# Optimization experiments

Hardware: AMD Instinct MI355X
Metric: run time of the kernel (lower is better)

## Reference

```python
import jax, jax.numpy as jnp
import numpy as np
import math

N, C_S, C_Z, C_IPA, H, NQ, NV = 768, 384, 128, 16, 12, 4, 8


def setup_inputs() -> dict:
    key = jax.random.key(0)
    ks = jax.random.split(key, 16)
    inp = {
        "s": jax.random.normal(ks[0], (N, C_S), jnp.float32),
        "z": jax.random.normal(ks[1], (N, N, C_Z), jnp.float32),
        "rots": jax.random.normal(ks[2], (N, 3, 3), jnp.float32),
        "trans": jax.random.normal(ks[3], (N, 3), jnp.float32),
        "mask": jnp.ones((N,), jnp.float32),
    }
    sc = 0.02
    inp["Wq"] = jax.random.normal(ks[4], (C_S, H * C_IPA), jnp.float32) * sc
    inp["bq"] = jnp.zeros((H * C_IPA,), jnp.float32)
    inp["Wkv"] = jax.random.normal(ks[5], (C_S, H * 2 * C_IPA), jnp.float32) * sc
    inp["bkv"] = jnp.zeros((H * 2 * C_IPA,), jnp.float32)
    inp["Wq3"] = jax.random.normal(ks[6], (C_S, H * 3 * NQ), jnp.float32) * sc
    inp["bq3"] = jnp.zeros((H * 3 * NQ,), jnp.float32)
    inp["Wkv3"] = jax.random.normal(ks[7], (C_S, H * 3 * (NQ + NV)), jnp.float32) * sc
    inp["bkv3"] = jnp.zeros((H * 3 * (NQ + NV),), jnp.float32)
    inp["Wb"] = jax.random.normal(ks[8], (C_Z, H), jnp.float32) * sc
    inp["bb"] = jnp.zeros((H,), jnp.float32)
    inp["hw"] = jnp.zeros((H,), jnp.float32)
    inp["Wo"] = jax.random.normal(ks[9], (H * (C_Z + C_IPA + NV * 4), C_S), jnp.float32) * sc
    inp["bo"] = jnp.zeros((C_S,), jnp.float32)
    return inp


def reference(s, z, rots, trans, mask, Wq, bq, Wkv, bkv, Wq3, bq3, Wkv3, bkv3, Wb, bb, hw, Wo, bo):
    normsize = math.sqrt(1.0 / (3 * C_IPA))
    normsize_B = math.sqrt(1.0 / 3.0)
    normsize_hw = math.sqrt(1.0 / (3 * NQ * 9.0 / 2))

    # scalar Q/K/V: [N, H, C_IPA]
    Q = (s @ Wq + bq).reshape(N, H, C_IPA)
    KV = (s @ Wkv + bkv).reshape(N, H, 2, C_IPA)
    K, V = KV[..., 0, :], KV[..., 1, :]

    # query points: project, place into global frame via rigid transform
    Q3 = (s @ Wq3 + bq3).reshape(N, 3, NQ * H).swapaxes(-1, -2)        # [N, NQ*H, 3]
    Q3 = jnp.einsum('nij,nkj->nki', rots, Q3) + trans[:, None, :]
    Q3 = Q3.reshape(N, H, NQ, 3)

    KV3 = (s @ Wkv3 + bkv3).reshape(N, 3, H * (NQ + NV)).swapaxes(-1, -2)
    KV3 = jnp.einsum('nij,nkj->nki', rots, KV3) + trans[:, None, :]
    KV3 = KV3.reshape(N, H, NQ + NV, 3)
    K3, V3 = KV3[:, :, :NQ, :], KV3[:, :, NQ:, :]                      # points per head

    # pair bias [N, N, H]
    B = z @ Wb + bb

    # scalar attention logits + pair bias
    AT = jnp.einsum('ihc,jhc->ijh', Q, K) * normsize + B * normsize_B

    # point attention: squared distances [N, N, H, NQ]
    d2 = jnp.sum(jnp.square(Q3[:, None] - K3[None, :]), axis=-1)
    hw_sp = jax.nn.softplus(hw) * normsize_hw                          # [H]
    AT3 = -0.5 * jnp.sum(d2 * hw_sp[None, None, :, None], axis=-1)     # [N, N, H]

    # mask bias: large negative where either residue masked out
    mask2 = mask[:, None] * mask[None, :]
    B3 = (mask2 - 1.0) * 1e9                                           # [N, N]

    AT = jax.nn.softmax(AT + AT3 + B3[..., None], axis=-2)             # softmax over j

    # scalar value aggregation
    O = jnp.einsum('ijh,jhc->ihc', AT, V).reshape(N, -1)

    # point value aggregation, then map back to local frame (inverse transform)
    O3 = jnp.einsum('ijh,jhcd->ihcd', AT, V3).reshape(N, H * NV, 3)
    O3 = jnp.einsum('nji,nkj->nki', rots, O3 - trans[:, None, :])      # rots^T @ (O3 - t)
    O3_norm = jnp.sqrt(jnp.sum(jnp.square(O3), axis=-1) + 1e-20)       # [N, H*NV]

    # pair representation aggregation
    O_pair = jnp.einsum('ijh,ijc->ihc', AT, z).reshape(N, -1)

    O_final = jnp.concatenate((O, O3[..., 0], O3[..., 1], O3[..., 2], O3_norm, O_pair), axis=-1)
    return O_final @ Wo + bo
```

## Files before the change

kernel.cpp:

```cpp
#include <hip/hip_runtime.h>
#include <cstdint>


typedef __attribute__((ext_vector_type(8))) short short8;
typedef __attribute__((ext_vector_type(4))) short short4_t;
typedef __attribute__((ext_vector_type(4))) float f32x4;

__device__ __forceinline__ unsigned short f2bf(float f) {
    unsigned u = __float_as_uint(f);
    u = (u + 0x7FFFu + ((u >> 16) & 1u)) >> 16;
    return (unsigned short)u;
}
__device__ __forceinline__ float bf2f(unsigned short s) {
    return __uint_as_float(((unsigned)s) << 16);
}
__device__ __forceinline__ unsigned pk2(float lo, float hi) {
    return (unsigned)f2bf(lo) | ((unsigned)f2bf(hi) << 16);
}
__device__ __forceinline__ int HOFF(int gg) {
    return gg * 6 + ((gg & 2) << 2);
}

__global__ __launch_bounds__(256) void proj_kernel(
    const float* __restrict__ s,
    const float* __restrict__ Wq,   const float* __restrict__ bq,
    const float* __restrict__ Wkv,  const float* __restrict__ bkv,
    const float* __restrict__ Wq3,  const float* __restrict__ bq3,
    const float* __restrict__ Wkv3, const float* __restrict__ bkv3,
    float* __restrict__ Qw, unsigned short* __restrict__ Kw,
    unsigned short* __restrict__ Vw,
    float* __restrict__ P3q, float* __restrict__ P3kv)
{
    __shared__ __align__(16) float s_lds[32 * 384];
    const int t  = threadIdx.x;
    const int r0 = blockIdx.x * 32;
    const int c0 = blockIdx.y * 128;

    for (int u = t; u < 3072; u += 256) {
        int r = u / 96, c4 = u - r * 96;
        *(float4*)&s_lds[r * 384 + c4 * 4] =
            *(const float4*)&s[(size_t)(r0 + r) * 384 + c4 * 4];
    }
    __syncthreads();

    const int rg = t >> 6;
    const int lc = t & 63;
    const int colA = c0 + lc;
    const int colB = c0 + lc + 64;

    const float *wpA, *wpB; int ldA, ldB; float biasA, biasB;
    {
        int col = colA;
        if (col < 192)      { wpA = Wq   + col;       ldA = 192; biasA = bq[col]; }
        else if (col < 576) { wpA = Wkv  + (col-192); ldA = 384; biasA = bkv[col-192]; }
        else if (col < 720) { wpA = Wq3  + (col-576); ldA = 144; biasA = bq3[col-576]; }
        else                { wpA = Wkv3 + (col-720); ldA = 432; biasA = bkv3[col-720]; }
        col = colB;
        if (col < 192)      { wpB = Wq   + col;       ldB = 192; biasB = bq[col]; }
        else if (col < 576) { wpB = Wkv  + (col-192); ldB = 384; biasB = bkv[col-192]; }
        else if (col < 720) { wpB = Wq3  + (col-576); ldB = 144; biasB = bq3[col-576]; }
        else                { wpB = Wkv3 + (col-720); ldB = 432; biasB = bkv3[col-720]; }
    }

    float acc0[8] = {}, acc1[8] = {};
    for (int k = 0; k < 384; k += 4) {
        float4 sv[8];
        #pragma unroll
        for (int r = 0; r < 8; r++)
            sv[r] = *(const float4*)&s_lds[(rg*8 + r) * 384 + k];
        #pragma unroll
        for (int kk = 0; kk < 4; kk++) {
            float w0 = wpA[(k + kk) * ldA];
            float w1 = wpB[(k + kk) * ldB];
            #pragma unroll
            for (int r = 0; r < 8; r++) {
                float sval = ((const float*)&sv[r])[kk];
                acc0[r] += sval * w0;
                acc1[r] += sval * w1;
            }
        }
    }

    #pragma unroll
    for (int q = 0; q < 2; q++) {
        int col   = q ? colB : colA;
        float bia = q ? biasB : biasA;
        #pragma unroll
        for (int r = 0; r < 8; r++) {
            int row = r0 + rg*8 + r;
            float v = (q ? acc1[r] : acc0[r]) + bia;
            if (col < 192) {
                Qw[(size_t)row*192 + col] = v;
            } else if (col < 576) {
                int c = col - 192, h = c >> 5, sub = c & 31;
                if (sub < 16) Kw[(size_t)row*192 + h*16 + sub]      = f2bf(v);
                else          Vw[(size_t)row*192 + h*16 + (sub-16)] = f2bf(v);
            } else if (col < 720) {
                P3q[(size_t)row*144 + (col-576)] = v;
            } else {
                P3kv[(size_t)row*432 + (col-720)] = v;
            }
        }
    }
}

__global__ __launch_bounds__(192) void rot3_kernel(
    const float* __restrict__ P3q, const float* __restrict__ P3kv,
    const float* __restrict__ rots, const float* __restrict__ trans,
    float* __restrict__ Q3w, unsigned short* __restrict__ K3w,
    unsigned short* __restrict__ V3w)
{
    const int n = blockIdx.x;
    const int t = threadIdx.x;
    float R[9];
    #pragma unroll
    for (int u = 0; u < 9; u++) R[u] = rots[n*9 + u];
    float T0 = trans[n*3+0], T1 = trans[n*3+1], T2 = trans[n*3+2];

    float p0, p1, p2;
    if (t < 48) {
        p0 = P3q[(size_t)n*144 + t];
        p1 = P3q[(size_t)n*144 + 48 + t];
        p2 = P3q[(size_t)n*144 + 96 + t];
    } else {
        int k = t - 48;
        p0 = P3kv[(size_t)n*432 + k];
        p1 = P3kv[(size_t)n*432 + 144 + k];
        p2 = P3kv[(size_t)n*432 + 288 + k];
    }
    float o0 = R[0]*p0 + R[1]*p1 + R[2]*p2 + T0;
    float o1 = R[3]*p0 + R[4]*p1 + R[5]*p2 + T1;
    float o2 = R[6]*p0 + R[7]*p1 + R[8]*p2 + T2;

    if (t < 48) {
        Q3w[(size_t)n*144 + t*3 + 0] = o0;
        Q3w[(size_t)n*144 + t*3 + 1] = o1;
        Q3w[(size_t)n*144 + t*3 + 2] = o2;
    } else {
        int k = t - 48, h = k / 12, m = k % 12;
        if (m < 4) {
            size_t base = (size_t)n*144 + (h*4 + m)*3;
            K3w[base+0] = f2bf(o0); K3w[base+1] = f2bf(o1); K3w[base+2] = f2bf(o2);
        } else {
            size_t base = (size_t)n*384 + (h*8 + (m-4))*4;
            V3w[base+0] = f2bf(o0); V3w[base+1] = f2bf(o1); V3w[base+2] = f2bf(o2);
        }
    }
}

__global__ __launch_bounds__(256, 4) void ipa_main(
    const float* __restrict__ z, const float* __restrict__ mask,
    const float* __restrict__ Wb, const float* __restrict__ bb,
    const float* __restrict__ hw,
    const float* __restrict__ Qw, const unsigned short* __restrict__ Kw,
    const unsigned short* __restrict__ Vw,
    const float* __restrict__ Q3w, const unsigned short* __restrict__ K3w,
    const unsigned short* __restrict__ V3w,
    float* __restrict__ part3)
{
    __shared__ __align__(16) unsigned short z_l[90 * 88];
    __shared__ __align__(16) unsigned short wbT_l[16 * 136];
    __shared__ __align__(16) float          p_l[32 * 17];
    __shared__ __align__(16) unsigned short pT_l[16 * 40];
    __shared__ __align__(16) float          Q_lds[192];
    __shared__ __align__(16) float          Q3_lds[144];
    __shared__ float hw_lds[12], bb_lds[12];

    const int i     = blockIdx.x >> 1;
    const int chunk = blockIdx.x & 1;
    const int t    = threadIdx.x;
    const int lane = t & 63;
    const int wv   = t >> 6;
    const int g    = lane >> 4;
    const int lm   = lane & 15;

    if (t < 192) Q_lds[t]  = Qw[(size_t)i*192 + t];
    if (t < 144) Q3_lds[t] = Q3w[(size_t)i*144 + t];
    if (t < 12) {
        hw_lds[t] = log1pf(__expf(hw[t])) * 0.13608276348795434f;
        bb_lds[t] = bb[t];
    }
    if (t < 160) pT_l[480 + t] = 0;
    for (int u = t; u < 1536; u += 256) {
        int h = u % 12, c = u / 12;
        wbT_l[h*136 + c] = f2bf(Wb[c*12 + h]);
    }
    const float mask_i = mask[i];

    f32x4 opA = {0,0,0,0}, opB = {0,0,0,0};
    float oacc = 0.0f;
    float o3x = 0, o3y = 0, o3z = 0;
    float dena = 0;
    const int oh = t >> 4, oc = t & 15;
    int o3h = -1, o3v = 0, o3j0 = 0, o3j1 = 32, o3slot = 0;
    if (t >= 192)    { o3h = (t - 192) >> 3;      o3v = (t - 192) & 7; }
    else if (t < 32) { o3h = 8 + (t >> 3);        o3v = t & 7;        o3j1 = 16; }
    else if (t < 64) { o3h = 8 + ((t - 32) >> 3); o3v = (t - 32) & 7; o3j0 = 16; o3slot = 1; }
    const int denh = (t >= 64 && t < 76) ? (t - 64) : -1;

    const int jj  = t >> 3, c16 = t & 7;
    const float* zbase = z + ((size_t)i*768 + chunk*384 + jj)*128 + c16*16;
    const int chS  = (jj >> 2)*8 + c16;
    const int chP  = chS + HOFF(chS >> 4);
    const int sidx = chP*88 + (jj & 3)*16;

    __syncthreads();

    for (int tile = 0; tile < 12; tile++) {
        const int j0 = chunk*384 + tile*32;

        {
            const float* zp = zbase + (size_t)tile * 32 * 128;
            float4 f0 = *(const float4*)(zp + 0);
            float4 f1 = *(const float4*)(zp + 4);
            float4 f2 = *(const float4*)(zp + 8);
            float4 f3 = *(const float4*)(zp + 12);
            uint4* dst = (uint4*)&z_l[sidx];
            dst[0] = uint4{pk2(f0.x,f0.y), pk2(f0.z,f0.w), pk2(f1.x,f1.y), pk2(f1.z,f1.w)};
            dst[1] = uint4{pk2(f2.x,f2.y), pk2(f2.z,f2.w), pk2(f3.x,f3.y), pk2(f3.z,f3.w)};
        }
        __syncthreads();

        if (wv < 2) {
            f32x4 ab = {0,0,0,0};
            const int jt = wv;
            #pragma unroll
            for (int ks = 0; ks < 4; ks++) {
                short8 bf = *(const short8*)&wbT_l[lm*136 + ks*32 + g*8];
                int jr = jt*16 + lm;
                int ch = (jr >> 2)*8 + ks*2 + (g >> 1);
                int cp = ch + HOFF(ch >> 4);
                short8 a = *(const short8*)&z_l[cp*88 + (jr & 3)*16 + (g & 1)*8];
                ab = __builtin_amdgcn_mfma_f32_16x16x32_bf16(a, bf, ab, 0, 0, 0);
            }
            if (lm < 12) {
                #pragma unroll
                for (int r = 0; r < 4; r++)
                    p_l[(jt*16 + g*4 + r)*17 + lm] = ab[r];
            }
        }
        __syncthreads();

        #pragma unroll
        for (int rep = 0; rep < 2; rep++) {
            int pr = t + rep*256;
            if (pr < 384) {
                int jjq = pr / 12;
                int h   = pr - jjq*12;
                int j   = j0 + jjq;
                float Bv = p_l[jjq*17 + h];
                const unsigned short* kp = Kw + (size_t)j*192 + h*16;
                short8 kA = *(const short8*)(kp);
                short8 kB = *(const short8*)(kp + 8);
                float qk = 0.0f;
                #pragma unroll
                for (int e = 0; e < 8; e++) qk += Q_lds[h*16 + e]     * bf2f((unsigned short)kA[e]);
                #pragma unroll
                for (int e = 0; e < 8; e++) qk += Q_lds[h*16 + 8 + e] * bf2f((unsigned short)kB[e]);
                const unsigned short* k3p = K3w + (size_t)j*144 + h*12;
                short4_t c0v = *(const short4_t*)(k3p);
                short4_t c1v = *(const short4_t*)(k3p + 4);
                short4_t c2v = *(const short4_t*)(k3p + 8);
                float d2 = 0.0f;
                #pragma unroll
                for (int e = 0; e < 4; e++) { float d = Q3_lds[h*12 + e]     - bf2f((unsigned short)c0v[e]); d2 += d*d; }
                #pragma unroll
                for (int e = 0; e < 4; e++) { float d = Q3_lds[h*12 + 4 + e] - bf2f((unsigned short)c1v[e]); d2 += d*d; }
                #pragma unroll
                for (int e = 0; e < 4; e++) { float d = Q3_lds[h*12 + 8 + e] - bf2f((unsigned short)c2v[e]); d2 += d*d; }
                float mj = mask[j];
                float lg = qk * 0.14433756729740643f
                         + (Bv + bb_lds[h]) * 0.5773502691896258f
                         - 0.5f * hw_lds[h] * d2
                         + (mask_i * mj - 1.0f) * 1e9f;
                float p = __expf(lg);
                p_l[jjq*17 + h]  = p;
                pT_l[h*40 + jjq] = f2bf(p);
            }
        }
        __syncthreads();

        {
            const int nt0 = wv*2;
            short8 ap = *(const short8*)((const char*)pT_l + lm*80 + g*16);
            short8 b0, b1;
            #pragma unroll
            for (int e = 0; e < 8; e++) {
                int jje = g*8 + e;
                int su  = (jje >> 2)*8;
                int ro  = (jje & 3)*16;
                int cp0 = su + nt0 + HOFF(g);
                b0[e] = (short)z_l[cp0*88 + ro + lm];
                b1[e] = (short)z_l[(cp0 + 1)*88 + ro + lm];
            }
            opA = __builtin_amdgcn_mfma_f32_16x16x32_bf16(ap, b0, opA, 0, 0, 0);
            opB = __builtin_amdgcn_mfma_f32_16x16x32_bf16(ap, b1, opB, 0, 0, 0);
        }
        if (t < 192) {
            #pragma unroll 8
            for (int jjq = 0; jjq < 32; jjq++) {
                float p = p_l[jjq*17 + oh];
                oacc += p * bf2f(Vw[(size_t)(j0 + jjq)*192 + oh*16 + oc]);
            }
        }
        if (o3h >= 0) {
            #pragma unroll 8
            for (int jjq = o3j0; jjq < o3j1; jjq++) {
                float p = p_l[jjq*17 + o3h];
                short4_t v4 = *(const short4_t*)(V3w + (size_t)(j0 + jjq)*384 + (o3h*8 + o3v)*4);
                o3x += p * bf2f((unsigned short)v4[0]);
                o3y += p * bf2f((unsigned short)v4[1]);
                o3z += p * bf2f((unsigned short)v4[2]);
            }
        }
        if (denh >= 0) {
            #pragma unroll 8
            for (int jjq = 0; jjq < 32; jjq++) dena += p_l[jjq*17 + denh];
        }
        __syncthreads();
    }

    float* pb = part3 + (size_t)blockIdx.x * 2560;
    if (t < 192) pb[t] = oacc;
    if (o3h >= 0) {
        int base = 192 + o3slot*288 + (o3h*8 + o3v)*3;
        pb[base+0] = o3x; pb[base+1] = o3y; pb[base+2] = o3z;
    }
    if (denh >= 0) pb[2304 + denh] = dena;
    {
        const int nt0 = wv*2;
        #pragma unroll
        for (int r = 0; r < 4; r++) {
            int h = g*4 + r;
            if (h < 12) {
                pb[768 + h*128 + nt0*16 + lm]       = opA[r];
                pb[768 + h*128 + (nt0 + 1)*16 + lm] = opB[r];
            }
        }
    }
}

__global__ __launch_bounds__(256) void combine_kernel(
    const float* __restrict__ part3, const float* __restrict__ rots,
    const float* __restrict__ trans, unsigned short* __restrict__ OF)
{
    const int i = blockIdx.x;
    const int t = threadIdx.x;
    const float* pa = part3 + (size_t)i*2*2560;
    const float* pb = pa + 2560;
    __shared__ float den_s[12];
    if (t < 12) den_s[t] = pa[2304 + t] + pb[2304 + t];
    __syncthreads();

    const size_t ofb = (size_t)i * 2112;
    if (t < 192) OF[ofb + t] = f2bf((pa[t] + pb[t]) / den_s[t >> 4]);
    if (t < 96) {
        int h = t >> 3, v = t & 7;
        float den = den_s[h];
        int base = 192 + t*3;
        float m0 = pa[base+0] + pb[base+0];
        float m1 = pa[base+1] + pb[base+1];
        float m2 = pa[base+2] + pb[base+2];
        if (h >= 8) {
            m0 += pa[base+288+0] + pb[base+288+0];
            m1 += pa[base+288+1] + pb[base+288+1];
            m2 += pa[base+288+2] + pb[base+288+2];
        }
        m0 = m0 / den - trans[i*3+0];
        m1 = m1 / den - trans[i*3+1];
        m2 = m2 / den - trans[i*3+2];
        const float* R = rots + (size_t)i*9;
        float r0v = R[0]*m0 + R[3]*m1 + R[6]*m2;
        float r1v = R[1]*m0 + R[4]*m1 + R[7]*m2;
        float r2v = R[2]*m0 + R[5]*m1 + R[8]*m2;
        float nrm = sqrtf(r0v*r0v + r1v*r1v + r2v*r2v + 1e-20f);
        int hv = h*8 + v;
        OF[ofb + 192 + hv] = f2bf(r0v);
        OF[ofb + 288 + hv] = f2bf(r1v);
        OF[ofb + 384 + hv] = f2bf(r2v);
        OF[ofb + 480 + hv] = f2bf(nrm);
    }
    for (int u = t; u < 1536; u += 256) {
        OF[ofb + 576 + u] = f2bf((pa[768 + u] + pb[768 + u]) / den_s[u >> 7]);
    }
}

__global__ __launch_bounds__(256) void out_gemm(
    const unsigned short* __restrict__ OF, const float* __restrict__ Wo,
    float* __restrict__ part)
{
    __shared__ __align__(16) float aT[32 * 132];
    __shared__ __align__(16) float bt[32 * 68];
    const int t  = threadIdx.x;
    const int i0 = blockIdx.x * 128;
    const int c0 = blockIdx.y * 64;
    const int k0 = blockIdx.z * 352;
    const int r0 = (t & 15) * 8;
    const int c4 = (t >> 4) * 4;

    float acc[8][4] = {};

    for (int kt = 0; kt < 11; kt++) {
        const int kk0 = k0 + kt*32;
        __syncthreads();
        {
            int r = t >> 1, kh = (t & 1) * 16;
            const unsigned short* apg = OF + (size_t)(i0 + r)*2112 + kk0 + kh;
            short8 v0 = *(const short8*)apg;
            short8 v1 = *(const short8*)(apg + 8);
            #pragma unroll
            for (int e = 0; e < 8; e++) aT[(kh + e)*132 + r]     = bf2f((unsigned short)v0[e]);
            #pragma unroll
            for (int e = 0; e < 8; e++) aT[(kh + 8 + e)*132 + r] = bf2f((unsigned short)v1[e]);
        }
        {
            int k = t >> 3, c8 = (t & 7) * 8;
            const float* wpg = Wo + (size_t)(kk0 + k)*384 + c0 + c8;
            *(float4*)&bt[k*68 + c8]     = *(const float4*)wpg;
            *(float4*)&bt[k*68 + c8 + 4] = *(const float4*)(wpg + 4);
        }
        __syncthreads();
        #pragma unroll 4
        for (int kk = 0; kk < 32; kk++) {
            float4 a0 = *(float4*)&aT[kk*132 + r0];
            float4 a1 = *(float4*)&aT[kk*132 + r0 + 4];
            float4 bv = *(float4*)&bt[kk*68 + c4];
            #pragma unroll
            for (int ci = 0; ci < 4; ci++) {
                float b = ((const float*)&bv)[ci];
                acc[0][ci] += ((const float*)&a0)[0] * b;
                acc[1][ci] += ((const float*)&a0)[1] * b;
                acc[2][ci] += ((const float*)&a0)[2] * b;
                acc[3][ci] += ((const float*)&a0)[3] * b;
                acc[4][ci] += ((const float*)&a1)[0] * b;
                acc[5][ci] += ((const float*)&a1)[1] * b;
                acc[6][ci] += ((const float*)&a1)[2] * b;
                acc[7][ci] += ((const float*)&a1)[3] * b;
            }
        }
    }

    float* pbv = part + (size_t)blockIdx.z * 294912;
    #pragma unroll
    for (int ri = 0; ri < 8; ri++) {
        float4 o = {acc[ri][0], acc[ri][1], acc[ri][2], acc[ri][3]};
        *(float4*)&pbv[(size_t)(i0 + r0 + ri)*384 + c0 + c4] = o;
    }
}

__global__ __launch_bounds__(256) void reduce_out(
    const float* __restrict__ part, const float* __restrict__ bo,
    float* __restrict__ out)
{
    int idx = blockIdx.x * 256 + threadIdx.x;
    float v = bo[idx % 384];
    #pragma unroll
    for (int s = 0; s < 6; s++) v += part[(size_t)s * 294912 + idx];
    out[idx] = v;
}

extern "C" void kernel_launch(void* const* d_in, const int* in_sizes, int n_in,
                              void* d_out, int out_size, void* d_ws, size_t ws_size,
                              hipStream_t stream) {
    const float* s     = (const float*)d_in[0];
    const float* z     = (const float*)d_in[1];
    const float* rots  = (const float*)d_in[2];
    const float* trans = (const float*)d_in[3];
    const float* mask  = (const float*)d_in[4];
    const float* Wq    = (const float*)d_in[5];
    const float* bq    = (const float*)d_in[6];
    const float* Wkv   = (const float*)d_in[7];
    const float* bkv   = (const float*)d_in[8];
    const float* Wq3   = (const float*)d_in[9];
    const float* bq3   = (const float*)d_in[10];
    const float* Wkv3  = (const float*)d_in[11];
    const float* bkv3  = (const float*)d_in[12];
    const float* Wb    = (const float*)d_in[13];
    const float* bb    = (const float*)d_in[14];
    const float* hw    = (const float*)d_in[15];
    const float* Wo    = (const float*)d_in[16];
    const float* bo    = (const float*)d_in[17];
    float* out = (float*)d_out;

    char* ws = (char*)d_ws;
    float*          Qw   = (float*)(ws + 0);
    float*          Q3w  = (float*)(ws + 589824);
    unsigned short* Kw   = (unsigned short*)(ws + 1032192);
    unsigned short* Vw   = (unsigned short*)(ws + 1327104);
    unsigned short* K3w  = (unsigned short*)(ws + 1622016);
    unsigned short* V3w  = (unsigned short*)(ws + 1843200);
    float*          P3q  = (float*)(ws + 2433024);
    float*          P3kv = (float*)(ws + 2875392);
    unsigned short* OF   = (unsigned short*)(ws + 4202496);
    float*          part3 = (float*)(ws + 7446528);
    float*          part  = (float*)(ws + 7446528);

    proj_kernel<<<dim3(24, 9), 256, 0, stream>>>(
        s, Wq, bq, Wkv, bkv, Wq3, bq3, Wkv3, bkv3, Qw, Kw, Vw, P3q, P3kv);
    rot3_kernel<<<768, 192, 0, stream>>>(P3q, P3kv, rots, trans, Q3w, K3w, V3w);
    ipa_main<<<1536, 256, 0, stream>>>(
        z, mask, Wb, bb, hw, Qw, Kw, Vw, Q3w, K3w, V3w, part3);
    combine_kernel<<<768, 256, 0, stream>>>(part3, rots, trans, OF);
    out_gemm<<<dim3(6, 6, 6), 256, 0, stream>>>(OF, Wo, part);
    reduce_out<<<1152, 256, 0, stream>>>(part, bo, out);
}
```

Measured before the change: 258.4 us.

## Fold logits into augmented Q/K dot product and pipeline z tiles with V aggregation

Adds an ek_kernel that builds 32-wide augmented query and key rows. Each row packs the scaled scalar q/k, the weighted point coordinates, the squared-norm terms, the bias and the mask terms, so each logit becomes a single dot product instead of separate qk, distance and mask evaluations. V and V3 are stored transposed so each thread reads contiguous j-runs. The main loop prefetches the next z tile into registers and runs the V/V3 aggregation for the previous tile on waves 2-3 while waves 0-1 compute the bias MFMA and the exponentials, using double-buffered probability buffers. The costs are an extra kernel launch, bf16 rounding of the augmented terms, and a mask encoded as a large bf16 constant whose error tolerance depends on S.

After: 473.0 us. 1.83x slower.

```diff
diff --git a/kernel.cpp b/kernel.cpp
--- a/kernel.cpp
+++ b/kernel.cpp
@@ -20,6 +20,10 @@
 __device__ __forceinline__ int HOFF(int gg) {
     return gg * 6 + ((gg & 2) << 2);
 }
+
+#define NS_QK  0.14433756729740643f
+#define NS_B   0.5773502691896258f
+#define NS_HW  0.13608276348795434f
 
 __global__ __launch_bounds__(256) void proj_kernel(
     const float* __restrict__ s,
@@ -28,7 +32,7 @@
     const float* __restrict__ Wq3,  const float* __restrict__ bq3,
     const float* __restrict__ Wkv3, const float* __restrict__ bkv3,
     float* __restrict__ Qw, unsigned short* __restrict__ Kw,
-    unsigned short* __restrict__ Vw,
+    unsigned short* __restrict__ Vt,
     float* __restrict__ P3q, float* __restrict__ P3kv)
 {
     __shared__ __align__(16) float s_lds[32 * 384];
@@ -93,8 +97,8 @@
                 Qw[(size_t)row*192 + col] = v;
             } else if (col < 576) {
                 int c = col - 192, h = c >> 5, sub = c & 31;
-                if (sub < 16) Kw[(size_t)row*192 + h*16 + sub]      = f2bf(v);
-                else          Vw[(size_t)row*192 + h*16 + (sub-16)] = f2bf(v);
+                if (sub < 16) Kw[(size_t)row*192 + h*16 + sub] = f2bf(v);
+                else          Vt[(size_t)(h*16 + (sub-16))*768 + row] = f2bf(v);
             } else if (col < 720) {
                 P3q[(size_t)row*144 + (col-576)] = v;
             } else {
@@ -107,8 +111,8 @@
 __global__ __launch_bounds__(192) void rot3_kernel(
     const float* __restrict__ P3q, const float* __restrict__ P3kv,
     const float* __restrict__ rots, const float* __restrict__ trans,
-    float* __restrict__ Q3w, unsigned short* __restrict__ K3w,
-    unsigned short* __restrict__ V3w)
+    float* __restrict__ Q3w, float* __restrict__ K3w,
+    unsigned short* __restrict__ V3t)
 {
     const int n = blockIdx.x;
     const int t = threadIdx.x;
@@ -140,31 +144,85 @@
         int k = t - 48, h = k / 12, m = k % 12;
         if (m < 4) {
             size_t base = (size_t)n*144 + (h*4 + m)*3;
-            K3w[base+0] = f2bf(o0); K3w[base+1] = f2bf(o1); K3w[base+2] = f2bf(o2);
+            K3w[base+0] = o0; K3w[base+1] = o1; K3w[base+2] = o2;
         } else {
-            size_t base = (size_t)n*384 + (h*8 + (m-4))*4;
-            V3w[base+0] = f2bf(o0); V3w[base+1] = f2bf(o1); V3w[base+2] = f2bf(o2);
-        }
+            int rv = (h*8 + (m-4))*3;
+            V3t[(size_t)(rv+0)*768 + n] = f2bf(o0);
+            V3t[(size_t)(rv+1)*768 + n] = f2bf(o1);
+            V3t[(size_t)(rv+2)*768 + n] = f2bf(o2);
+        }
+    }
+}
+
+__global__ __launch_bounds__(256) void ek_kernel(
+    const float* __restrict__ Qw, const unsigned short* __restrict__ Kw,
+    const float* __restrict__ Q3w, const float* __restrict__ K3w,
+    const float* __restrict__ mask, const float* __restrict__ hw,
+    const float* __restrict__ bb,
+    unsigned short* __restrict__ EQw, unsigned short* __restrict__ EKw)
+{
+    const int idx = blockIdx.x * 4 + (threadIdx.x >> 6);
+    const int h   = threadIdx.x & 63;
+    if (h >= 12) return;
+    const float hws = log1pf(__expf(hw[h])) * NS_HW;
+    const float mi  = mask[idx];
+    const float S   = 31616.0f;
+
+    unsigned short row[32];
+    {
+        const unsigned short* kp = Kw + (size_t)idx*192 + h*16;
+        #pragma unroll
+        for (int c = 0; c < 16; c++) row[c] = kp[c];
+        const float* k3 = K3w + (size_t)idx*144 + h*12;
+        float kn = 0.0f;
+        #pragma unroll
+        for (int e = 0; e < 12; e++) {
+            unsigned short b = f2bf(k3[e]);
+            row[16+e] = b;
+            float f = bf2f(b); kn += f*f;
+        }
+        row[28] = f2bf(bb[h]*NS_B - 0.5f*hws*kn);
+        row[29] = f2bf(1.0f);
+        row[30] = f2bf(mi * S);
+        row[31] = f2bf(-S);
+        unsigned short* o = EKw + ((size_t)idx*12 + h)*32;
+        #pragma unroll
+        for (int c = 0; c < 32; c++) o[c] = row[c];
+    }
+    {
+        const float* qp = Qw + (size_t)idx*192 + h*16;
+        #pragma unroll
+        for (int c = 0; c < 16; c++) row[c] = f2bf(qp[c] * NS_QK);
+        const float* q3 = Q3w + (size_t)idx*144 + h*12;
+        float qn = 0.0f;
+        #pragma unroll
+        for (int e = 0; e < 12; e++) {
+            float f = q3[e];
+            row[16+e] = f2bf(f * hws);
+            qn += f*f;
+        }
+        row[28] = f2bf(1.0f);
+        row[29] = f2bf(-0.5f*hws*qn);
+        row[30] = f2bf(mi * S);
+        row[31] = f2bf(S);
+        unsigned short* o = EQw + ((size_t)idx*12 + h)*32;
+        #pragma unroll
+        for (int c = 0; c < 32; c++) o[c] = row[c];
     }
 }
 
 __global__ __launch_bounds__(256, 4) void ipa_main(
-    const float* __restrict__ z, const float* __restrict__ mask,
-    const float* __restrict__ Wb, const float* __restrict__ bb,
-    const float* __restrict__ hw,
-    const float* __restrict__ Qw, const unsigned short* __restrict__ Kw,
-    const unsigned short* __restrict__ Vw,
-    const float* __restrict__ Q3w, const unsigned short* __restrict__ K3w,
-    const unsigned short* __restrict__ V3w,
+    const float* __restrict__ z,
+    const float* __restrict__ Wb,
+    const unsigned short* __restrict__ EQw, const unsigned short* __restrict__ EKw,
+    const unsigned short* __restrict__ Vt, const unsigned short* __restrict__ V3t,
     float* __restrict__ part3)
 {
     __shared__ __align__(16) unsigned short z_l[90 * 88];
+    __shared__ __align__(16) float          p_l[2][32 * 17];
+    __shared__ __align__(16) unsigned short pT_l[2][16 * 40];
+    __shared__ __align__(16) float          eq_l[12 * 33];
     __shared__ __align__(16) unsigned short wbT_l[16 * 136];
-    __shared__ __align__(16) float          p_l[32 * 17];
-    __shared__ __align__(16) unsigned short pT_l[16 * 40];
-    __shared__ __align__(16) float          Q_lds[192];
-    __shared__ __align__(16) float          Q3_lds[144];
-    __shared__ float hw_lds[12], bb_lds[12];
 
     const int i     = blockIdx.x >> 1;
     const int chunk = blockIdx.x & 1;
@@ -174,29 +232,17 @@
     const int g    = lane >> 4;
     const int lm   = lane & 15;
 
-    if (t < 192) Q_lds[t]  = Qw[(size_t)i*192 + t];
-    if (t < 144) Q3_lds[t] = Q3w[(size_t)i*144 + t];
-    if (t < 12) {
-        hw_lds[t] = log1pf(__expf(hw[t])) * 0.13608276348795434f;
-        bb_lds[t] = bb[t];
-    }
-    if (t < 160) pT_l[480 + t] = 0;
+    for (int u = t; u < 384; u += 256) {
+        int h = u >> 5, c = u & 31;
+        eq_l[h*33 + c] = bf2f(EQw[((size_t)i*12 + h)*32 + c]);
+    }
     for (int u = t; u < 1536; u += 256) {
         int h = u % 12, c = u / 12;
         wbT_l[h*136 + c] = f2bf(Wb[c*12 + h]);
     }
-    const float mask_i = mask[i];
-
-    f32x4 opA = {0,0,0,0}, opB = {0,0,0,0};
-    float oacc = 0.0f;
-    float o3x = 0, o3y = 0, o3z = 0;
-    float dena = 0;
-    const int oh = t >> 4, oc = t & 15;
-    int o3h = -1, o3v = 0, o3j0 = 0, o3j1 = 32, o3slot = 0;
-    if (t >= 192)    { o3h = (t - 192) >> 3;      o3v = (t - 192) & 7; }
-    else if (t < 32) { o3h = 8 + (t >> 3);        o3v = t & 7;        o3j1 = 16; }
-    else if (t < 64) { o3h = 8 + ((t - 32) >> 3); o3v = (t - 32) & 7; o3j0 = 16; o3slot = 1; }
-    const int denh = (t >= 64 && t < 76) ? (t - 64) : -1;
+    for (int u = t; u < 512; u += 256)
+        wbT_l[(12 + (u >> 7))*136 + (u & 127)] = 0;
+    if (t < 160) { pT_l[0][480 + t] = 0; pT_l[1][480 + t] = 0; }
 
     const int jj  = t >> 3, c16 = t & 7;
     const float* zbase = z + ((size_t)i*768 + chunk*384 + jj)*128 + c16*16;
@@ -204,85 +250,137 @@
     const int chP  = chS + HOFF(chS >> 4);
     const int sidx = chP*88 + (jj & 3)*16;
 
+    f32x4 opA = {0,0,0,0}, opB = {0,0,0,0};
+    float oa = 0, ob = 0, oc2 = 0;
+    float o3x = 0, o3y = 0, o3z = 0;
+    float dn = 0;
+    const int w = t - 128;
+
+    {
+        float4 f0 = *(const float4*)(zbase + 0);
+        float4 f1 = *(const float4*)(zbase + 4);
+        float4 f2 = *(const float4*)(zbase + 8);
+        float4 f3 = *(const float4*)(zbase + 12);
+        uint4* dst = (uint4*)&z_l[sidx];
+        dst[0] = uint4{pk2(f0.x,f0.y), pk2(f0.z,f0.w), pk2(f1.x,f1.y), pk2(f1.z,f1.w)};
+        dst[1] = uint4{pk2(f2.x,f2.y), pk2(f2.z,f2.w), pk2(f3.x,f3.y), pk2(f3.z,f3.w)};
+    }
     __syncthreads();
 
+    auto vwork = [&](int tt) {
+        const int j0v = chunk*384 + tt*32;
+        const float* pp = p_l[tt & 1];
+        if (w < 96) {
+            short8 va[4];
+            #pragma unroll
+            for (int q = 0; q < 4; q++)
+                va[q] = *(const short8*)(Vt + (size_t)w*768 + j0v + q*8);
+            short8 v3[3][4];
+            #pragma unroll
+            for (int d = 0; d < 3; d++)
+                #pragma unroll
+                for (int q = 0; q < 4; q++)
+                    v3[d][q] = *(const short8*)(V3t + (size_t)(w*3 + d)*768 + j0v + q*8);
+            const int ohp = w >> 4, o3hp = w >> 3;
+            #pragma unroll
+            for (int j2 = 0; j2 < 32; j2++) {
+                float p1 = pp[j2*17 + ohp];
+                oa += p1 * bf2f((unsigned short)va[j2>>3][j2&7]);
+                float pv = pp[j2*17 + o3hp];
+                o3x += pv * bf2f((unsigned short)v3[0][j2>>3][j2&7]);
+                o3y += pv * bf2f((unsigned short)v3[1][j2>>3][j2&7]);
+                o3z += pv * bf2f((unsigned short)v3[2][j2>>3][j2&7]);
+            }
+        } else {
+            short8 va[4], vb[4], vc[4];
+            #pragma unroll
+            for (int q = 0; q < 4; q++) {
+                va[q] = *(const short8*)(Vt + (size_t)w*768      + j0v + q*8);
+                vb[q] = *(const short8*)(Vt + (size_t)(w+32)*768 + j0v + q*8);
+                vc[q] = *(const short8*)(Vt + (size_t)(w+64)*768 + j0v + q*8);
+            }
+            const int ha = w >> 4, hb = ha + 2, hc = ha + 4;
+            #pragma unroll
+            for (int j2 = 0; j2 < 32; j2++) {
+                oa  += pp[j2*17 + ha] * bf2f((unsigned short)va[j2>>3][j2&7]);
+                ob  += pp[j2*17 + hb] * bf2f((unsigned short)vb[j2>>3][j2&7]);
+                oc2 += pp[j2*17 + hc] * bf2f((unsigned short)vc[j2>>3][j2&7]);
+            }
+        }
+    };
+
     for (int tile = 0; tile < 12; tile++) {
-        const int j0 = chunk*384 + tile*32;
-
-        {
-            const float* zp = zbase + (size_t)tile * 32 * 128;
-            float4 f0 = *(const float4*)(zp + 0);
-            float4 f1 = *(const float4*)(zp + 4);
-            float4 f2 = *(const float4*)(zp + 8);
-            float4 f3 = *(const float4*)(zp + 12);
-            uint4* dst = (uint4*)&z_l[sidx];
-            dst[0] = uint4{pk2(f0.x,f0.y), pk2(f0.z,f0.w), pk2(f1.x,f1.y), pk2(f1.z,f1.w)};
-            dst[1] = uint4{pk2(f2.x,f2.y), pk2(f2.z,f2.w), pk2(f3.x,f3.y), pk2(f3.z,f3.w)};
-        }
-        __syncthreads();
+        const int j0  = chunk*384 + tile*32;
+        const int cur = tile & 1, prv = cur ^ 1;
+        const bool more = (tile < 11);
+
+        float4 zf0, zf1, zf2, zf3;
+        if (more) {
+            const float* zp = zbase + (size_t)(tile + 1) * 4096;
+            zf0 = *(const float4*)(zp + 0);
+            zf1 = *(const float4*)(zp + 4);
+            zf2 = *(const float4*)(zp + 8);
+            zf3 = *(const float4*)(zp + 12);
+        }
 
         if (wv < 2) {
             f32x4 ab = {0,0,0,0};
-            const int jt = wv;
             #pragma unroll
             for (int ks = 0; ks < 4; ks++) {
                 short8 bf = *(const short8*)&wbT_l[lm*136 + ks*32 + g*8];
-                int jr = jt*16 + lm;
+                int jr = wv*16 + lm;
                 int ch = (jr >> 2)*8 + ks*2 + (g >> 1);
                 int cp = ch + HOFF(ch >> 4);
                 short8 a = *(const short8*)&z_l[cp*88 + (jr & 3)*16 + (g & 1)*8];
                 ab = __builtin_amdgcn_mfma_f32_16x16x32_bf16(a, bf, ab, 0, 0, 0);
             }
             if (lm < 12) {
+                const float* eqh = eq_l + lm*33;
                 #pragma unroll
-                for (int r = 0; r < 4; r++)
-                    p_l[(jt*16 + g*4 + r)*17 + lm] = ab[r];
-            }
-        }
-        __syncthreads();
-
-        #pragma unroll
-        for (int rep = 0; rep < 2; rep++) {
-            int pr = t + rep*256;
-            if (pr < 384) {
-                int jjq = pr / 12;
-                int h   = pr - jjq*12;
-                int j   = j0 + jjq;
-                float Bv = p_l[jjq*17 + h];
-                const unsigned short* kp = Kw + (size_t)j*192 + h*16;
-                short8 kA = *(const short8*)(kp);
-                short8 kB = *(const short8*)(kp + 8);
-                float qk = 0.0f;
+                for (int r = 0; r < 4; r++) {
+                    int jl = wv*16 + g*4 + r;
+                    int j  = j0 + jl;
+                    const unsigned short* ek = EKw + ((size_t)j*12 + lm)*32;
+                    short8 e0 = *(const short8*)(ek);
+                    short8 e1 = *(const short8*)(ek + 8);
+                    short8 e2 = *(const short8*)(ek + 16);
+                    short8 e3 = *(const short8*)(ek + 24);
+                    float acc = ab[r] * NS_B;
+                    #pragma unroll
+                    for (int c = 0; c < 8; c++) acc += eqh[c]      * bf2f((unsigned short)e0[c]);
+                    #pragma unroll
+                    for (int c = 0; c < 8; c++) acc += eqh[8 + c]  * bf2f((unsigned short)e1[c]);
+                    #pragma unroll
+                    for (int c = 0; c < 8; c++) acc += eqh[16 + c] * bf2f((unsigned short)e2[c]);
+                    #pragma unroll
+                    for (int c = 0; c < 6; c++) acc += eqh[24 + c] * bf2f((unsigned short)e3[c]);
+                    float mterm = eqh[30] * bf2f((unsigned short)e3[6]);
+                    mterm += eqh[31] * bf2f((unsigned short)e3[7]);
+                    acc += mterm;
+                    float p = __expf(acc);
+                    p_l[cur][jl*17 + lm]  = p;
+                    pT_l[cur][lm*40 + jl] = f2bf(p);
+                }
+            } else if (wv == 0 && lm < 15 && tile > 0) {
+                const int dh = g*3 + (lm - 12);
+                const float* pp = p_l[prv];
                 #pragma unroll
-                for (int e = 0; e < 8; e++) qk += Q_lds[h*16 + e]     * bf2f((unsigned short)kA[e]);
-                #pragma unroll
-                for (int e = 0; e < 8; e++) qk += Q_lds[h*16 + 8 + e] * bf2f((unsigned short)kB[e]);
-                const unsigned short* k3p = K3w + (size_t)j*144 + h*12;
-                short4_t c0v = *(const short4_t*)(k3p);
-                short4_t c1v = *(const short4_t*)(k3p + 4);
-                short4_t c2v = *(const short4_t*)(k3p + 8);
-                float d2 = 0.0f;
-                #pragma unroll
-                for (int e = 0; e < 4; e++) { float d = Q3_lds[h*12 + e]     - bf2f((unsigned short)c0v[e]); d2 += d*d; }
-                #pragma unroll
-                for (int e = 0; e < 4; e++) { float d = Q3_lds[h*12 + 4 + e] - bf2f((unsigned short)c1v[e]); d2 += d*d; }
-                #pragma unroll
-                for (int e = 0; e < 4; e++) { float d = Q3_lds[h*12 + 8 + e] - bf2f((unsigned short)c2v[e]); d2 += d*d; }
-                float mj = mask[j];
-                float lg = qk * 0.14433756729740643f
-                         + (Bv + bb_lds[h]) * 0.5773502691896258f
-                         - 0.5f * hw_lds[h] * d2
-                         + (mask_i * mj - 1.0f) * 1e9f;
-                float p = __expf(lg);
-                p_l[jjq*17 + h]  = p;
-                pT_l[h*40 + jjq] = f2bf(p);
-            }
+                for (int j2 = 0; j2 < 32; j2++) dn += pp[j2*17 + dh];
+            }
+        } else {
+            if (tile > 0) vwork(tile - 1);
+        }
+
+        uint4 s0, s1;
+        if (more) {
+            s0 = uint4{pk2(zf0.x,zf0.y), pk2(zf0.z,zf0.w), pk2(zf1.x,zf1.y), pk2(zf1.z,zf1.w)};
+            s1 = uint4{pk2(zf2.x,zf2.y), pk2(zf2.z,zf2.w), pk2(zf3.x,zf3.y), pk2(zf3.z,zf3.w)};
         }
         __syncthreads();
 
         {
             const int nt0 = wv*2;
-            short8 ap = *(const short8*)((const char*)pT_l + lm*80 + g*16);
+            short8 ap = *(const short8*)((const char*)pT_l[cur] + lm*80 + g*16);
             short8 b0, b1;
             #pragma unroll
             for (int e = 0; e < 8; e++) {
@@ -296,37 +394,36 @@
             opA = __builtin_amdgcn_mfma_f32_16x16x32_bf16(ap, b0, opA, 0, 0, 0);
             opB = __builtin_amdgcn_mfma_f32_16x16x32_bf16(ap, b1, opB, 0, 0, 0);
         }
-        if (t < 192) {
-            #pragma unroll 8
-            for (int jjq = 0; jjq < 32; jjq++) {
-                float p = p_l[jjq*17 + oh];
-                oacc += p * bf2f(Vw[(size_t)(j0 + jjq)*192 + oh*16 + oc]);
-            }
-        }
-        if (o3h >= 0) {
-            #pragma unroll 8
-            for (int jjq = o3j0; jjq < o3j1; jjq++) {
-                float p = p_l[jjq*17 + o3h];
-                short4_t v4 = *(const short4_t*)(V3w + (size_t)(j0 + jjq)*384 + (o3h*8 + o3v)*4);
-                o3x += p * bf2f((unsigned short)v4[0]);
-                o3y += p * bf2f((unsigned short)v4[1]);
-                o3z += p * bf2f((unsigned short)v4[2]);
-            }
-        }
-        if (denh >= 0) {
-            #pragma unroll 8
-            for (int jjq = 0; jjq < 32; jjq++) dena += p_l[jjq*17 + denh];
-        }
         __syncthreads();
+
+        if (more) {
+            uint4* dst = (uint4*)&z_l[sidx];
+            dst[0] = s0; dst[1] = s1;
+        }
+        __syncthreads();
+    }
+
+    if (wv >= 2) vwork(11);
+    if (wv == 0 && lm >= 12 && lm < 15) {
+        const int dh = g*3 + (lm - 12);
+        const float* pp = p_l[1];
+        #pragma unroll
+        for (int j2 = 0; j2 < 32; j2++) dn += pp[j2*17 + dh];
     }
 
     float* pb = part3 + (size_t)blockIdx.x * 2560;
-    if (t < 192) pb[t] = oacc;
-    if (o3h >= 0) {
-        int base = 192 + o3slot*288 + (o3h*8 + o3v)*3;
-        pb[base+0] = o3x; pb[base+1] = o3y; pb[base+2] = o3z;
-    }
-    if (denh >= 0) pb[2304 + denh] = dena;
+    if (wv >= 2) {
+        pb[w] = oa;
+        if (w < 96) {
+            pb[192 + w*3 + 0] = o3x;
+            pb[192 + w*3 + 1] = o3y;
+            pb[192 + w*3 + 2] = o3z;
+        } else {
+            pb[w + 32] = ob;
+            pb[w + 64] = oc2;
+        }
+    }
+    if (wv == 0 && lm >= 12 && lm < 15) pb[2304 + g*3 + (lm - 12)] = dn;
     {
         const int nt0 = wv*2;
         #pragma unroll
@@ -358,17 +455,9 @@
         int h = t >> 3, v = t & 7;
         float den = den_s[h];
         int base = 192 + t*3;
-        float m0 = pa[base+0] + pb[base+0];
-        float m1 = pa[base+1] + pb[base+1];
-        float m2 = pa[base+2] + pb[base+2];
-        if (h >= 8) {
-            m0 += pa[base+288+0] + pb[base+288+0];
-            m1 += pa[base+288+1] + pb[base+288+1];
-            m2 += pa[base+288+2] + pb[base+288+2];
-        }
-        m0 = m0 / den - trans[i*3+0];
-        m1 = m1 / den - trans[i*3+1];
-        m2 = m2 / den - trans[i*3+2];
+        float m0 = (pa[base+0] + pb[base+0]) / den - trans[i*3+0];
+        float m1 = (pa[base+1] + pb[base+1]) / den - trans[i*3+1];
+        float m2 = (pa[base+2] + pb[base+2]) / den - trans[i*3+2];
         const float* R = rots + (size_t)i*9;
         float r0v = R[0]*m0 + R[3]*m1 + R[6]*m2;
         float r1v = R[1]*m0 + R[4]*m1 + R[7]*m2;
@@ -486,20 +575,22 @@
     float*          Qw   = (float*)(ws + 0);
     float*          Q3w  = (float*)(ws + 589824);
     unsigned short* Kw   = (unsigned short*)(ws + 1032192);
-    unsigned short* Vw   = (unsigned short*)(ws + 1327104);
-    unsigned short* K3w  = (unsigned short*)(ws + 1622016);
-    unsigned short* V3w  = (unsigned short*)(ws + 1843200);
-    float*          P3q  = (float*)(ws + 2433024);
-    float*          P3kv = (float*)(ws + 2875392);
-    unsigned short* OF   = (unsigned short*)(ws + 4202496);
-    float*          part3 = (float*)(ws + 7446528);
-    float*          part  = (float*)(ws + 7446528);
+    unsigned short* Vt   = (unsigned short*)(ws + 1327104);
+    float*          K3w  = (float*)(ws + 1622016);
+    unsigned short* V3t  = (unsigned short*)(ws + 2064384);
+    float*          P3q  = (float*)(ws + 2506752);
+    float*          P3kv = (float*)(ws + 2949120);
+    unsigned short* EQw  = (unsigned short*)(ws + 4276224);
+    unsigned short* EKw  = (unsigned short*)(ws + 4866048);
+    unsigned short* OF   = (unsigned short*)(ws + 5455872);
+    float*          part3 = (float*)(ws + 8699904);
+    float*          part  = (float*)(ws + 8699904);
 
     proj_kernel<<<dim3(24, 9), 256, 0, stream>>>(
-        s, Wq, bq, Wkv, bkv, Wq3, bq3, Wkv3, bkv3, Qw, Kw, Vw, P3q, P3kv);
-    rot3_kernel<<<768, 192, 0, stream>>>(P3q, P3kv, rots, trans, Q3w, K3w, V3w);
-    ipa_main<<<1536, 256, 0, stream>>>(
-        z, mask, Wb, bb, hw, Qw, Kw, Vw, Q3w, K3w, V3w, part3);
+        s, Wq, bq, Wkv, bkv, Wq3, bq3, Wkv3, bkv3, Qw, Kw, Vt, P3q, P3kv);
+    rot3_kernel<<<768, 192, 0, stream>>>(P3q, P3kv, rots, trans, Q3w, K3w, V3t);
+    ek_kernel<<<192, 256, 0, stream>>>(Qw, Kw, Q3w, K3w, mask, hw, bb, EQw, EKw);
+    ipa_main<<<1536, 256, 0, stream>>>(z, Wb, EQw, EKw, Vt, V3t, part3);
     combine_kernel<<<768, 256, 0, stream>>>(part3, rots, trans, OF);
     out_gemm<<<dim3(6, 6, 6), 256, 0, stream>>>(OF, Wo, part);
     reduce_out<<<1152, 256, 0, stream>>>(part, bo, out);
```

## Replace FP32 output GEMM and split-K reduce with bf16 MFMA GEMM

Applied to the files above, without the earlier changes.

The scalar FP32 split-K output projection and its separate reduction kernel are replaced by a single bf16 MFMA GEMM that adds the bias directly into the output. A new per-call kernel first converts Wo to a transposed bf16 copy so both operands can be streamed as contiguous 8-element K vectors. The new GEMM reads operands straight from global memory with no LDS staging and launches only 72 blocks. It also adds an extra launch, lowers Wo precision to bf16, and may underuse the GPU.

Result: slower. 270.0 us (+4.5%).

```diff
diff --git a/kernel.cpp b/kernel.cpp
--- a/kernel.cpp
+++ b/kernel.cpp
@@ -385,78 +385,64 @@
     }
 }
 
-__global__ __launch_bounds__(256) void out_gemm(
-    const unsigned short* __restrict__ OF, const float* __restrict__ Wo,
-    float* __restrict__ part)
-{
-    __shared__ __align__(16) float aT[32 * 132];
-    __shared__ __align__(16) float bt[32 * 68];
-    const int t  = threadIdx.x;
-    const int i0 = blockIdx.x * 128;
-    const int c0 = blockIdx.y * 64;
-    const int k0 = blockIdx.z * 352;
-    const int r0 = (t & 15) * 8;
-    const int c4 = (t >> 4) * 4;
-
-    float acc[8][4] = {};
-
-    for (int kt = 0; kt < 11; kt++) {
-        const int kk0 = k0 + kt*32;
-        __syncthreads();
-        {
-            int r = t >> 1, kh = (t & 1) * 16;
-            const unsigned short* apg = OF + (size_t)(i0 + r)*2112 + kk0 + kh;
-            short8 v0 = *(const short8*)apg;
-            short8 v1 = *(const short8*)(apg + 8);
-            #pragma unroll
-            for (int e = 0; e < 8; e++) aT[(kh + e)*132 + r]     = bf2f((unsigned short)v0[e]);
-            #pragma unroll
-            for (int e = 0; e < 8; e++) aT[(kh + 8 + e)*132 + r] = bf2f((unsigned short)v1[e]);
-        }
-        {
-            int k = t >> 3, c8 = (t & 7) * 8;
-            const float* wpg = Wo + (size_t)(kk0 + k)*384 + c0 + c8;
-            *(float4*)&bt[k*68 + c8]     = *(const float4*)wpg;
-            *(float4*)&bt[k*68 + c8 + 4] = *(const float4*)(wpg + 4);
-        }
-        __syncthreads();
-        #pragma unroll 4
-        for (int kk = 0; kk < 32; kk++) {
-            float4 a0 = *(float4*)&aT[kk*132 + r0];
-            float4 a1 = *(float4*)&aT[kk*132 + r0 + 4];
-            float4 bv = *(float4*)&bt[kk*68 + c4];
-            #pragma unroll
-            for (int ci = 0; ci < 4; ci++) {
-                float b = ((const float*)&bv)[ci];
-                acc[0][ci] += ((const float*)&a0)[0] * b;
-                acc[1][ci] += ((const float*)&a0)[1] * b;
-                acc[2][ci] += ((const float*)&a0)[2] * b;
-                acc[3][ci] += ((const float*)&a0)[3] * b;
-                acc[4][ci] += ((const float*)&a1)[0] * b;
-                acc[5][ci] += ((const float*)&a1)[1] * b;
-                acc[6][ci] += ((const float*)&a1)[2] * b;
-                acc[7][ci] += ((const float*)&a1)[3] * b;
-            }
-        }
-    }
-
-    float* pbv = part + (size_t)blockIdx.z * 294912;
+__global__ __launch_bounds__(256) void wot_kernel(
+    const float* __restrict__ Wo, unsigned short* __restrict__ WoT)
+{
+    int id = blockIdx.x * 256 + threadIdx.x;
+    int c  = id % 384;
+    int k8 = id / 384;
+    unsigned short tmp[8];
     #pragma unroll
-    for (int ri = 0; ri < 8; ri++) {
-        float4 o = {acc[ri][0], acc[ri][1], acc[ri][2], acc[ri][3]};
-        *(float4*)&pbv[(size_t)(i0 + r0 + ri)*384 + c0 + c4] = o;
-    }
-}
-
-__global__ __launch_bounds__(256) void reduce_out(
-    const float* __restrict__ part, const float* __restrict__ bo,
-    float* __restrict__ out)
-{
-    int idx = blockIdx.x * 256 + threadIdx.x;
-    float v = bo[idx % 384];
+    for (int e = 0; e < 8; e++)
+        tmp[e] = f2bf(Wo[(size_t)(k8*8 + e)*384 + c]);
+    uint4 o;
+    o.x = (unsigned)tmp[0] | ((unsigned)tmp[1] << 16);
+    o.y = (unsigned)tmp[2] | ((unsigned)tmp[3] << 16);
+    o.z = (unsigned)tmp[4] | ((unsigned)tmp[5] << 16);
+    o.w = (unsigned)tmp[6] | ((unsigned)tmp[7] << 16);
+    *(uint4*)&WoT[(size_t)c*2112 + k8*8] = o;
+}
+
+__global__ __launch_bounds__(256) void out_gemm2(
+    const unsigned short* __restrict__ OF, const unsigned short* __restrict__ WoT,
+    const float* __restrict__ bo, float* __restrict__ out)
+{
+    const int t = threadIdx.x;
+    const int wv = t >> 6, lane = t & 63, g = lane >> 4, lm = lane & 15;
+    const int i0 = blockIdx.x * 32;
+    const int c0 = blockIdx.y * 128 + wv * 32;
+
+    f32x4 acc00 = {0,0,0,0}, acc01 = {0,0,0,0};
+    f32x4 acc10 = {0,0,0,0}, acc11 = {0,0,0,0};
+
+    const unsigned short* a0p = OF  + (size_t)(i0 + lm)*2112      + g*8;
+    const unsigned short* a1p = OF  + (size_t)(i0 + 16 + lm)*2112 + g*8;
+    const unsigned short* b0p = WoT + (size_t)(c0 + lm)*2112      + g*8;
+    const unsigned short* b1p = WoT + (size_t)(c0 + 16 + lm)*2112 + g*8;
+
+    #pragma unroll 2
+    for (int k = 0; k < 2112; k += 32) {
+        short8 a0 = *(const short8*)(a0p + k);
+        short8 a1 = *(const short8*)(a1p + k);
+        short8 b0 = *(const short8*)(b0p + k);
+        short8 b1 = *(const short8*)(b1p + k);
+        acc00 = __builtin_amdgcn_mfma_f32_16x16x32_bf16(a0, b0, acc00, 0, 0, 0);
+        acc01 = __builtin_amdgcn_mfma_f32_16x16x32_bf16(a0, b1, acc01, 0, 0, 0);
+        acc10 = __builtin_amdgcn_mfma_f32_16x16x32_bf16(a1, b0, acc10, 0, 0, 0);
+        acc11 = __builtin_amdgcn_mfma_f32_16x16x32_bf16(a1, b1, acc11, 0, 0, 0);
+    }
+
+    const int colA = c0 + lm, colB = c0 + 16 + lm;
+    const float bA = bo[colA], bB = bo[colB];
     #pragma unroll
-    for (int s = 0; s < 6; s++) v += part[(size_t)s * 294912 + idx];
-    out[idx] = v;
+    for (int r = 0; r < 4; r++) {
+        int rowA = i0 + g*4 + r;
+        int rowB = i0 + 16 + g*4 + r;
+        out[(size_t)rowA*384 + colA] = acc00[r] + bA;
+        out[(size_t)rowA*384 + colB] = acc01[r] + bB;
+        out[(size_t)rowB*384 + colA] = acc10[r] + bA;
+        out[(size_t)rowB*384 + colB] = acc11[r] + bB;
+    }
 }
 
 extern "C" void kernel_launch(void* const* d_in, const int* in_sizes, int n_in,
@@ -493,14 +479,14 @@
     float*          P3kv = (float*)(ws + 2875392);
     unsigned short* OF   = (unsigned short*)(ws + 4202496);
     float*          part3 = (float*)(ws + 7446528);
-    float*          part  = (float*)(ws + 7446528);
-
+    unsigned short* WoT  = (unsigned short*)(ws + 23175168);
+
+    wot_kernel<<<396, 256, 0, stream>>>(Wo, WoT);
     proj_kernel<<<dim3(24, 9), 256, 0, stream>>>(
         s, Wq, bq, Wkv, bkv, Wq3, bq3, Wkv3, bkv3, Qw, Kw, Vw, P3q, P3kv);
     rot3_kernel<<<768, 192, 0, stream>>>(P3q, P3kv, rots, trans, Q3w, K3w, V3w);
     ipa_main<<<1536, 256, 0, stream>>>(
         z, mask, Wb, bb, hw, Qw, Kw, Vw, Q3w, K3w, V3w, part3);
     combine_kernel<<<768, 256, 0, stream>>>(part3, rots, trans, OF);
-    out_gemm<<<dim3(6, 6, 6), 256, 0, stream>>>(OF, Wo, part);
-    reduce_out<<<1152, 256, 0, stream>>>(part, bo, out);
-}
+    out_gemm2<<<dim3(24, 3), 256, 0, stream>>>(OF, WoT, bo, out);
+}
```
